# Kernel tuning notes

Hardware: AMD Instinct MI355X
Metric: run time of the kernel (lower is better)

The kernel has to match this reference:

```python
import jax, jax.numpy as jnp
import numpy as np

HID, HEADS, NL, WIN = 512, 4, 2, 5
DH = HID // HEADS
SLOPE = 0.2
EPS = 1e-5
B, L = 16, 1024
NEG_INF = -1e30


def _layer_norm(x, g, b):
    m = jnp.mean(x, axis=-1, keepdims=True)
    v = jnp.mean(jnp.square(x - m), axis=-1, keepdims=True)
    return (x - m) * jax.lax.rsqrt(v + EPS) * g + b


def _build_masks(attention_mask, last_starts, seq_len):
    # node layout: [g, h_1..h_T, l], total N = seq_len + 2
    bsz = attention_mask.shape[0]
    N = seq_len + 2
    pos = jnp.arange(N)
    last = last_starts[:, None, None]  # (B,1,1)
    global_mask = jnp.ones((bsz, 1, N), jnp.float32)
    # local node: g, itself, and tokens of the last utterance (node idx last+1 .. seq_len)
    local_mask = ((pos == 0) | (pos == N - 1) | ((pos >= last + 1) & (pos <= seq_len))).astype(jnp.float32)  # (B,1,N)
    # token nodes: global node + window of neighboring tokens
    ii = jnp.arange(seq_len)[:, None]          # query token index
    jj = jnp.arange(N)[None, :]                # key node index
    t = jj - 1                                 # token index of key node (valid in [0, seq_len))
    win = (t >= 0) & (t < seq_len) & (jnp.abs(ii - t) <= WIN)
    base = (jj == 0) | win                     # (L,N)
    # tokens at/after last utterance start also attend to the local node
    to_local = (jnp.arange(seq_len)[None, :, None] >= last_starts[:, None, None]) & (jj[None] == N - 1)  # (B,L,N)
    token_mask = (base[None] | to_local).astype(jnp.float32)
    # padding: key tokens masked by attention_mask; g and l always visible; padded queries fully masked
    ones_col = jnp.ones((bsz, seq_len, 1), jnp.float32)
    pad = jnp.concatenate([ones_col, jnp.broadcast_to(attention_mask[:, None, :], (bsz, seq_len, seq_len)), ones_col], axis=-1)
    token_mask = token_mask * pad * attention_mask[:, :, None]
    return global_mask, local_mask, token_mask


def _gat(q, kv, W, a, mask):
    # W: (hid, hid) as torch Linear weight (out,in); a: (H, 2*DH)
    bsz, Lq, _ = q.shape
    N = kv.shape[1]
    Q = (q @ W.T).reshape(bsz, Lq, HEADS, DH)
    K = (kv @ W.T).reshape(bsz, N, HEADS, DH)
    V = K  # key==value tensor in this module, same projection
    # additive score decomposes: (a . [Q||K]) = Q.a_q + K.a_k
    sq = jnp.einsum('bqhd,hd->bhq', Q, a[:, :DH])
    sk = jnp.einsum('bkhd,hd->bhk', K, a[:, DH:])
    s = sq[:, :, :, None] + sk[:, :, None, :]           # (B,H,Lq,N)
    s = jnp.where(s >= 0, s, SLOPE * s)                 # LeakyReLU
    s = jnp.where(mask[:, None, :, :] > 0, s, NEG_INF)
    w = jax.nn.softmax(s, axis=-1)
    w = jnp.where(jnp.isnan(w), 0.0, w)
    out = jnp.einsum('bhqk,bkhd->bqhd', w, V)
    return out.reshape(bsz, Lq, HID)


def setup_inputs() -> dict:
    key = jax.random.key(0)
    ks = jax.random.split(key, 10)
    scale = 1.0 / np.sqrt(HID)
    return {
        'global_embedding': jax.random.normal(ks[0], (B, HID), jnp.float32),
        'token_embeddings': jax.random.normal(ks[1], (B, L, HID), jnp.float32),
        'local_embedding': jax.random.normal(ks[2], (B, HID), jnp.float32),
        'attention_mask': jnp.ones((B, L), jnp.float32),
        'last_utterance_starts': jax.random.randint(ks[3], (B,), 0, 512, jnp.int32),
        'gat_W': jax.random.normal(ks[4], (NL, HID, HID), jnp.float32) * scale,
        'gat_a': jax.random.normal(ks[5], (NL, HEADS, 2 * DH), jnp.float32) * scale,
        'ln_gamma': jnp.ones((NL, HID), jnp.float32),
        'ln_beta': jnp.zeros((NL, HID), jnp.float32),
        'ffn_w1': jax.random.normal(ks[6], (3, HID, 4 * HID), jnp.float32) * scale,
        'ffn_b1': jnp.zeros((3, 4 * HID), jnp.float32),
        'ffn_w2': jax.random.normal(ks[7], (3, 4 * HID, HID), jnp.float32) * (1.0 / np.sqrt(4 * HID)),
        'ffn_b2': jnp.zeros((3, HID), jnp.float32),
        'out_ln_gamma': jnp.ones((3, HID), jnp.float32),
        'out_ln_beta': jnp.zeros((3, HID), jnp.float32),
    }


def reference(global_embedding, token_embeddings, local_embedding, attention_mask,
              last_utterance_starts, gat_W, gat_a, ln_gamma, ln_beta,
              ffn_w1, ffn_b1, ffn_w2, ffn_b2, out_ln_gamma, out_ln_beta):
    bsz, seq_len, _ = token_embeddings.shape
    gm, lm, tm = _build_masks(attention_mask, last_utterance_starts, seq_len)
    g = global_embedding[:, None, :]
    h = token_embeddings
    l = local_embedding[:, None, :]
    nodes = jnp.concatenate([g, h, l], axis=1)
    for k in range(NL):
        g_new = jax.nn.elu(_gat(g, nodes, gat_W[k], gat_a[k], gm))
        h_new = jax.nn.elu(_gat(h, nodes, gat_W[k], gat_a[k], tm))
        l_new = jax.nn.elu(_gat(l, nodes, gat_W[k], gat_a[k], lm))
        g = _layer_norm(g + g_new, ln_gamma[k], ln_beta[k])
        h = _layer_norm(h + h_new, ln_gamma[k], ln_beta[k])
        l = _layer_norm(l + l_new, ln_gamma[k], ln_beta[k])
        nodes = jnp.concatenate([g, h, l], axis=1)
    def ffn(x, i):
        hmid = jax.nn.gelu(x @ ffn_w1[i] + ffn_b1[i], approximate=False)
        return hmid @ ffn_w2[i] + ffn_b2[i]
    g = g + ffn(g, 0)
    h = h + ffn(h, 1)
    l = l + ffn(l, 2)
    updated_global = _layer_norm(g[:, 0], out_ln_gamma[0], out_ln_beta[0])
    updated_tokens = _layer_norm(h, out_ln_gamma[1], out_ln_beta[1])
    updated_local = _layer_norm(l[:, 0], out_ln_gamma[2], out_ln_beta[2])
    return updated_global, updated_tokens, updated_local
```

## Files before the change

### kernel.cpp

```cpp
#include <hip/hip_runtime.h>
#include <stdint.h>
#include <math.h>

#define HIDN 512
#define NHEAD 4
#define DHEAD 128
#define BATCH 16
#define SEQ 1024
#define NNODE 1026
#define MROWS (BATCH * NNODE)
#define MPAD 16512
#define MTOK (BATCH * SEQ)
#define FFD 2048
#define JCH 114

typedef short bf16x8 __attribute__((ext_vector_type(8)));
typedef float f32x4 __attribute__((ext_vector_type(4)));

__device__ __forceinline__ float bf2f(ushort u) {
    union { uint32_t i; float f; } v; v.i = ((uint32_t)u) << 16; return v.f;
}
__device__ __forceinline__ ushort f2bf(float f) {
    uint32_t x = __float_as_uint(f);
    return (ushort)((x + 0x7fffu + ((x >> 16) & 1u)) >> 16);
}
__device__ __forceinline__ float gelu(float v) {
    float z = v * 0.70710678118654752f;
    float az = fabsf(z);
    float t = __builtin_amdgcn_rcpf(1.f + 0.3275911f * az);
    float y = ((((1.061405429f * t - 1.453152027f) * t + 1.421413741f) * t
                - 0.284496736f) * t + 0.254829592f) * t;
    float e = __expf(-az * az);
    float erfv = 1.f - y * e;
    erfv = (z >= 0.f) ? erfv : -erfv;
    return 0.5f * v * (1.f + erfv);
}
__device__ __forceinline__ int cswz(int row, int col) {
    return row * 128 + ((((col >> 2) ^ (row & 7)) & 31) << 2) + (col & 3);
}

__global__ __launch_bounds__(256) void k_build_nodes(
    const float* __restrict__ g, const float* __restrict__ tok,
    const float* __restrict__ l, ushort* __restrict__ nb)
{
    int idx = blockIdx.x * 256 + threadIdx.x;
    int r = idx >> 9, c = idx & 511;
    float u = 0.f;
    if (r < MROWS) {
        int b = r / NNODE;
        int n = r - b * NNODE;
        if (n == 0)            u = g[b * HIDN + c];
        else if (n <= SEQ)     u = tok[((size_t)b * SEQ + (n - 1)) * HIDN + c];
        else                   u = l[b * HIDN + c];
    }
    nb[idx] = f2bf(u);
}

__global__ __launch_bounds__(256) void k_cvt(
    const float* __restrict__ in, ushort* __restrict__ out, int n)
{
    int idx = blockIdx.x * 256 + threadIdx.x;
    if (idx < n) out[idx] = f2bf(in[idx]);
}

__global__ __launch_bounds__(256) void k_transpose(
    const float* __restrict__ in, ushort* __restrict__ out, int R, int C)
{
    __shared__ float t[32][33];
    int x = blockIdx.x * 32 + threadIdx.x;
    int y0 = blockIdx.y * 32;
    for (int dy = threadIdx.y; dy < 32; dy += 8)
        t[dy][threadIdx.x] = in[(size_t)(y0 + dy) * C + x];
    __syncthreads();
    int ox = y0 + threadIdx.x;
    int oy0 = blockIdx.x * 32;
    for (int dy = threadIdx.y; dy < 32; dy += 8)
        out[(size_t)(oy0 + dy) * R + ox] = f2bf(t[threadIdx.x][dy]);
}

#define BM 128
#define BN 128
#define BK 64

__global__ __launch_bounds__(256) void k_gemm_bt(
    const ushort* __restrict__ A, const ushort* __restrict__ Bt,
    float* __restrict__ Cf, ushort* __restrict__ Cb,
    const float* __restrict__ bias,
    int N, int K, int ldb, int mode, int amap, int mguard, int first)
{
    __shared__ ushort smem[2 * (BM * BK + BN * BK)];
    int tid = threadIdx.x;
    int lane = tid & 63;
    int wave = tid >> 6;
    int wm = wave >> 1, wn = wave & 1;

    int GX = gridDim.x;
    int nwg = GX * gridDim.y;
    int bid = blockIdx.y * GX + blockIdx.x;
    int q = nwg >> 3, r = nwg & 7;
    int xcd = bid & 7, pos = bid >> 3;
    int cbase = (xcd < r) ? xcd * (q + 1) : r * (q + 1) + (xcd - r) * q;
    int wk = cbase + pos;
    int m0 = (wk / GX) * BM;
    int n0 = (wk % GX) * BN;

    f32x4 acc[4][4];
#pragma unroll
    for (int i = 0; i < 4; ++i)
#pragma unroll
        for (int j = 0; j < 4; ++j) acc[i][j] = (f32x4){0.f, 0.f, 0.f, 0.f};

    int lr = lane >> 3;
    int gco = ((lane & 7) ^ lr) * 8;

    const ushort* pA[4];
    const ushort* pB[4];
#pragma unroll
    for (int u = 0; u < 4; ++u) {
        int qq = wave * 4 + u;
        int rr8 = qq * 8 + lr;
        int grA = m0 + rr8;
        if (amap) grA = grA + 2 * (grA >> 10) + 1;
        pA[u] = A + (size_t)grA * K + gco;
        int grB = n0 + rr8;
        pB[u] = Bt + (size_t)grB * ldb + gco;
    }

    auto stage = [&](int buf) {
        ushort* sA = smem + buf * (BM * BK + BN * BK);
        ushort* sB = sA + BM * BK;
#pragma unroll
        for (int u = 0; u < 4; ++u) {
            int qq = wave * 4 + u;
            __builtin_amdgcn_global_load_lds(
                (const __attribute__((address_space(1))) void*)pA[u],
                (__attribute__((address_space(3))) void*)&sA[qq * 512], 16, 0, 0);
            __builtin_amdgcn_global_load_lds(
                (const __attribute__((address_space(1))) void*)pB[u],
                (__attribute__((address_space(3))) void*)&sB[qq * 512], 16, 0, 0);
            pA[u] += BK;
            pB[u] += BK;
        }
    };

    const int nk = K / BK;
    stage(0);
    __syncthreads();

    int rr = lane & 7;
    int rhi = (lane & 15) >> 3;
    for (int t = 0; t < nk; ++t) {
        if (t + 1 < nk) stage((t + 1) & 1);

        const ushort* sAr = smem + (t & 1) * (BM * BK + BN * BK);
        const ushort* sBr = sAr + BM * BK;
#pragma unroll
        for (int kk = 0; kk < BK; kk += 32) {
            int c4 = (kk >> 3) + (lane >> 4);
            int swz = rr * 64 + ((c4 ^ rr) << 3);
            bf16x8 af[4], bfr[4];
#pragma unroll
            for (int i = 0; i < 4; ++i)
                af[i] = *reinterpret_cast<const bf16x8*>(&sAr[(wm * 8 + i * 2 + rhi) * 512 + swz]);
#pragma unroll
            for (int j = 0; j < 4; ++j)
                bfr[j] = *reinterpret_cast<const bf16x8*>(&sBr[(wn * 8 + j * 2 + rhi) * 512 + swz]);
#pragma unroll
            for (int i = 0; i < 4; ++i)
#pragma unroll
                for (int j = 0; j < 4; ++j)
                    acc[i][j] = __builtin_amdgcn_mfma_f32_16x16x32_bf16(af[i], bfr[j], acc[i][j], 0, 0, 0);
        }
        asm volatile("s_waitcnt vmcnt(0)" ::: "memory");
        __builtin_amdgcn_s_barrier();
    }
    __syncthreads();

    float* sC = (float*)smem;
    int rb = (lane >> 4) * 4;
    int cb = lane & 15;
    int lrow = tid >> 2;
    int lcol = (tid & 3) << 5;
#pragma unroll
    for (int pass = 0; pass < 2; ++pass) {
        if (wm == pass) {
#pragma unroll
            for (int i = 0; i < 4; ++i)
#pragma unroll
                for (int j = 0; j < 4; ++j)
#pragma unroll
                    for (int rg = 0; rg < 4; ++rg)
                        sC[cswz(i * 16 + rb + rg, wn * 64 + j * 16 + cb)] = acc[i][j][rg];
        }
        __syncthreads();
        int gm = m0 + pass * 64 + lrow;
        if (gm < mguard) {
            int gn0 = n0 + lcol;
            float v[32];
#pragma unroll
            for (int e4 = 0; e4 < 8; ++e4) {
                float4 t = *(const float4*)&sC[cswz(lrow, lcol + e4 * 4)];
                v[e4 * 4 + 0] = t.x; v[e4 * 4 + 1] = t.y;
                v[e4 * 4 + 2] = t.z; v[e4 * 4 + 3] = t.w;
            }
            if (mode == 1 || mode == 3) {
                uint4* dst = (uint4*)(Cb + (size_t)gm * N + gn0);
#pragma unroll
                for (int q2 = 0; q2 < 4; ++q2) {
                    float s[8];
#pragma unroll
                    for (int t = 0; t < 8; ++t) {
                        float x = v[q2 * 8 + t];
                        s[t] = (mode == 1) ? gelu(x + bias[gn0 + q2 * 8 + t]) : x;
                    }
                    uint4 w;
                    w.x = (uint32_t)f2bf(s[0]) | ((uint32_t)f2bf(s[1]) << 16);
                    w.y = (uint32_t)f2bf(s[2]) | ((uint32_t)f2bf(s[3]) << 16);
                    w.z = (uint32_t)f2bf(s[4]) | ((uint32_t)f2bf(s[5]) << 16);
                    w.w = (uint32_t)f2bf(s[6]) | ((uint32_t)f2bf(s[7]) << 16);
                    dst[q2] = w;
                }
            } else {
                float4* dst = (float4*)(Cf + (size_t)gm * N + gn0);
#pragma unroll
                for (int e4 = 0; e4 < 8; ++e4) {
                    float4 t;
                    t.x = v[e4 * 4 + 0]; t.y = v[e4 * 4 + 1];
                    t.z = v[e4 * 4 + 2]; t.w = v[e4 * 4 + 3];
                    if (!first) {
                        float4 o = dst[e4];
                        t.x += o.x; t.y += o.y; t.z += o.z; t.w += o.w;
                    }
                    dst[e4] = t;
                }
            }
        }
        __syncthreads();
    }
}

__global__ __launch_bounds__(256) void k_sqsk(
    const ushort* __restrict__ P, const float* __restrict__ a,
    float* __restrict__ sq, float* __restrict__ sk)
{
    int wave = threadIdx.x >> 6, lane = threadIdx.x & 63;
    int row = blockIdx.x * 4 + wave;
    if (row >= MROWS) return;
    int hh = lane >> 4;
    int o0 = lane * 8;
    int dl = o0 & 127;
    const ushort* p = P + (size_t)row * HIDN + o0;
    const float* a1 = a + hh * 256 + dl;
    const float* a2 = a1 + 128;
    float s1 = 0.f, s2 = 0.f;
#pragma unroll
    for (int d = 0; d < 8; ++d) {
        float pv = bf2f(p[d]);
        s1 += pv * a1[d];
        s2 += pv * a2[d];
    }
#pragma unroll
    for (int off = 8; off; off >>= 1) {
        s1 += __shfl_xor(s1, off);
        s2 += __shfl_xor(s2, off);
    }
    if ((lane & 15) == 0) {
        sq[row * 4 + hh] = s1;
        sk[row * 4 + hh] = s2;
    }
}

__global__ __launch_bounds__(64) void k_attn_token(
    const ushort* __restrict__ P, const float* __restrict__ sq, const float* __restrict__ sk,
    const float* __restrict__ am, const int* __restrict__ last,
    const float* __restrict__ gam, const float* __restrict__ bet,
    ushort* __restrict__ nb)
{
    int bid = blockIdx.x;
    int tokid = ((bid & 7) << 11) | (bid >> 3);
    int b = tokid >> 10, i = tokid & 1023;
    int lane = threadIdx.x;
    int hh = lane >> 4;
    int base = b * NNODE;
    int qrow = base + 1 + i;

    int kr[13];
    int val[13];
    int rowok = am[b * SEQ + i] > 0.f ? 1 : 0;
    kr[0] = base; val[0] = rowok;
#pragma unroll
    for (int s = 0; s < 11; ++s) {
        int t = i - 5 + s;
        int inb = (t >= 0) && (t <= SEQ - 1);
        int tt = inb ? t : 0;
        int v = inb && rowok && (am[b * SEQ + tt] > 0.f);
        kr[1 + s] = base + 1 + tt;
        val[1 + s] = v;
    }
    kr[12] = base + SEQ + 1;
    val[12] = (rowok && (i >= last[b])) ? 1 : 0;

    float sqv = sq[qrow * 4 + hh];
    float sc[13];
    float mx = -1e30f;
#pragma unroll
    for (int t = 0; t < 13; ++t) {
        float s = 0.f;
        if (val[t]) {
            s = sqv + sk[kr[t] * 4 + hh];
            s = s >= 0.f ? s : 0.2f * s;
            mx = fmaxf(mx, s);
        }
        sc[t] = s;
    }
    float den = 0.f;
#pragma unroll
    for (int t = 0; t < 13; ++t) {
        float ev = 0.f;
        if (val[t]) ev = expf(sc[t] - mx);
        sc[t] = ev; den += ev;
    }
    float inv = (den > 1e-30f && den < 1e30f) ? 1.f / den : 0.f;

    int o0 = lane * 8;
    float accv[8] = {0.f, 0.f, 0.f, 0.f, 0.f, 0.f, 0.f, 0.f};
#pragma unroll
    for (int t = 0; t < 13; ++t) {
        if (val[t]) {
            float wgt = sc[t] * inv;
            const ushort* pv = P + (size_t)kr[t] * HIDN + o0;
#pragma unroll
            for (int d = 0; d < 8; ++d) accv[d] += wgt * bf2f(pv[d]);
        }
    }

    ushort* nrow = nb + (size_t)qrow * HIDN + o0;
    float x[8], s1 = 0.f, s2 = 0.f;
#pragma unroll
    for (int d = 0; d < 8; ++d) {
        float v = accv[d];
        v = v > 0.f ? v : expf(v) - 1.f;
        v += bf2f(nrow[d]);
        x[d] = v; s1 += v; s2 += v * v;
    }
#pragma unroll
    for (int off = 32; off; off >>= 1) { s1 += __shfl_xor(s1, off); s2 += __shfl_xor(s2, off); }
    float mean = s1 * (1.f / 512.f);
    float var = s2 * (1.f / 512.f) - mean * mean; var = fmaxf(var, 0.f);
    float rn = rsqrtf(var + 1e-5f);
#pragma unroll
    for (int d = 0; d < 8; ++d) {
        float y = (x[d] - mean) * rn * gam[o0 + d] + bet[o0 + d];
        nrow[d] = f2bf(y);
    }
}

__global__ __launch_bounds__(256) void k_glsm(
    const float* __restrict__ sq, const float* __restrict__ sk,
    const int* __restrict__ last,
    float* __restrict__ ebuf, float* __restrict__ einv)
{
    __shared__ float red[1024];
    int rw = blockIdx.x, b = rw >> 1, isl = rw & 1;
    int base = b * NNODE;
    int qrow = base + (isl ? (SEQ + 1) : 0);
    int lastb = last[b];
    int tid = threadIdx.x;

    float sqh[4];
#pragma unroll
    for (int h = 0; h < 4; ++h) sqh[h] = sq[qrow * 4 + h];

    float mx[4] = {-1e30f, -1e30f, -1e30f, -1e30f};
    for (int j = tid; j < NNODE; j += 256) {
        bool ok = !isl || (j == 0 || j == SEQ + 1 || (j >= lastb + 1 && j <= SEQ));
        if (ok) {
#pragma unroll
            for (int h = 0; h < 4; ++h) {
                float s = sqh[h] + sk[(base + j) * 4 + h];
                s = s >= 0.f ? s : 0.2f * s;
                mx[h] = fmaxf(mx[h], s);
            }
        }
    }
#pragma unroll
    for (int h = 0; h < 4; ++h) red[tid * 4 + h] = mx[h];
    __syncthreads();
    for (int s = 128; s; s >>= 1) {
        if (tid < s) {
#pragma unroll
            for (int h = 0; h < 4; ++h)
                red[tid * 4 + h] = fmaxf(red[tid * 4 + h], red[(tid + s) * 4 + h]);
        }
        __syncthreads();
    }
#pragma unroll
    for (int h = 0; h < 4; ++h) mx[h] = red[h];
    __syncthreads();

    float sm[4] = {0.f, 0.f, 0.f, 0.f};
    for (int j = tid; j < NNODE; j += 256) {
        bool ok = !isl || (j == 0 || j == SEQ + 1 || (j >= lastb + 1 && j <= SEQ));
#pragma unroll
        for (int h = 0; h < 4; ++h) {
            float v = 0.f;
            if (ok) {
                float s = sqh[h] + sk[(base + j) * 4 + h];
                s = s >= 0.f ? s : 0.2f * s;
                v = expf(s - mx[h]);
            }
            ebuf[((size_t)rw * NNODE + j) * 4 + h] = v;
            sm[h] += v;
        }
    }
#pragma unroll
    for (int h = 0; h < 4; ++h) red[tid * 4 + h] = sm[h];
    __syncthreads();
    for (int s = 128; s; s >>= 1) {
        if (tid < s) {
#pragma unroll
            for (int h = 0; h < 4; ++h) red[tid * 4 + h] += red[(tid + s) * 4 + h];
        }
        __syncthreads();
    }
    if (tid < 4) {
        float den = red[tid];
        einv[rw * 4 + tid] = (den > 1e-30f && den < 1e30f) ? 1.f / den : 0.f;
    }
}

__global__ __launch_bounds__(256) void k_glpv(
    const ushort* __restrict__ P, const float* __restrict__ ebuf,
    float* __restrict__ pout2)
{
    __shared__ float es[JCH * 4];
    int p = blockIdx.x, rw = blockIdx.y;
    int b = rw >> 1;
    int base = b * NNODE;
    int tid = threadIdx.x;
    for (int t = tid; t < JCH * 4; t += 256)
        es[t] = ebuf[((size_t)rw * NNODE + p * JCH) * 4 + t];
    __syncthreads();
    int o0 = tid, o1 = tid + 256;
    int h0 = o0 >> 7, h1 = o1 >> 7;
    const ushort* Pb = P + (size_t)(base + p * JCH) * HIDN;
    float a0 = 0.f, a1 = 0.f;
    for (int j = 0; j < JCH; ++j) {
        const ushort* pr = Pb + (size_t)j * HIDN;
        a0 += es[j * 4 + h0] * bf2f(pr[o0]);
        a1 += es[j * 4 + h1] * bf2f(pr[o1]);
    }
    float* o = pout2 + ((size_t)rw * 9 + p) * HIDN;
    o[o0] = a0;
    o[o1] = a1;
}

__global__ __launch_bounds__(256) void k_glred(
    const float* __restrict__ pout2, const float* __restrict__ einv,
    const float* __restrict__ gam, const float* __restrict__ bet,
    ushort* __restrict__ nb)
{
    __shared__ float red[512];
    int rw = blockIdx.x, b = rw >> 1, isl = rw & 1;
    size_t qrow = (size_t)b * NNODE + (isl ? SEQ + 1 : 0);
    int tid = threadIdx.x;
    float xv[2], s1 = 0.f, s2 = 0.f;
#pragma unroll
    for (int u = 0; u < 2; ++u) {
        int o = tid + u * 256;
        int h = o >> 7;
        float acc = 0.f;
#pragma unroll
        for (int p = 0; p < 9; ++p)
            acc += pout2[((size_t)rw * 9 + p) * HIDN + o];
        acc *= einv[rw * 4 + h];
        float v = acc > 0.f ? acc : expf(acc) - 1.f;
        v += bf2f(nb[qrow * HIDN + o]);
        xv[u] = v; s1 += v; s2 += v * v;
    }
    red[tid] = s1;
    __syncthreads();
    for (int s = 128; s; s >>= 1) { if (tid < s) red[tid] += red[tid + s]; __syncthreads(); }
    float mean = red[0] * (1.f / 512.f);
    __syncthreads();
    red[tid] = s2;
    __syncthreads();
    for (int s = 128; s; s >>= 1) { if (tid < s) red[tid] += red[tid + s]; __syncthreads(); }
    float var = red[0] * (1.f / 512.f) - mean * mean; var = fmaxf(var, 0.f);
    float rn = rsqrtf(var + 1e-5f);
#pragma unroll
    for (int u = 0; u < 2; ++u) {
        int o = tid + u * 256;
        float y = (xv[u] - mean) * rn * gam[o] + bet[o];
        nb[qrow * HIDN + o] = f2bf(y);
    }
}

__global__ __launch_bounds__(256) void k_fgl1(
    const ushort* __restrict__ nb, const float* __restrict__ w1,
    float* __restrict__ pmid)
{
    __shared__ float xs[64];
    int p = blockIdx.x, rw = blockIdx.y;
    int b = rw >> 1, isl = rw & 1;
    int idx = isl ? 2 : 0;
    size_t nrow = (size_t)b * NNODE + (isl ? SEQ + 1 : 0);
    int tid = threadIdx.x;
    if (tid < 64) xs[tid] = bf2f(nb[nrow * HIDN + p * 64 + tid]);
    __syncthreads();
    const float* W1 = w1 + (size_t)idx * HIDN * FFD + (size_t)p * 64 * FFD;
    float acc[8] = {0.f, 0.f, 0.f, 0.f, 0.f, 0.f, 0.f, 0.f};
    for (int ii = 0; ii < 64; ++ii) {
        float xv = xs[ii];
        const float* wrow = W1 + (size_t)ii * FFD + tid;
#pragma unroll
        for (int u = 0; u < 8; ++u) acc[u] += xv * wrow[u * 256];
    }
    float* o = pmid + ((size_t)rw * 8 + p) * FFD + tid;
#pragma unroll
    for (int u = 0; u < 8; ++u) o[u * 256] = acc[u];
}

__global__ __launch_bounds__(256) void k_fgl2(
    const float* __restrict__ pmid, const float* __restrict__ b1,
    float* __restrict__ mid)
{
    int g = blockIdx.x * 256 + threadIdx.x;
    int e4 = g * 4;
    int rw = e4 >> 11;
    int m = e4 & 2047;
    int isl = rw & 1;
    int idx = isl ? 2 : 0;
#pragma unroll
    for (int d = 0; d < 4; ++d) {
        float s = 0.f;
#pragma unroll
        for (int p = 0; p < 8; ++p)
            s += pmid[((size_t)rw * 8 + p) * FFD + m + d];
        s += b1[idx * FFD + m + d];
        mid[(size_t)rw * FFD + m + d] = gelu(s);
    }
}

__global__ __launch_bounds__(256) void k_fgl3(
    const float* __restrict__ mid, const float* __restrict__ w2,
    float* __restrict__ pout)
{
    __shared__ float ms[256];
    int p = blockIdx.x, rw = blockIdx.y;
    int isl = rw & 1;
    int idx = isl ? 2 : 0;
    int tid = threadIdx.x;
    ms[tid] = mid[(size_t)rw * FFD + p * 256 + tid];
    __syncthreads();
    const float* W2 = w2 + (size_t)idx * FFD * HIDN + (size_t)p * 256 * HIDN;
    float a0 = 0.f, a1 = 0.f;
    for (int mm = 0; mm < 256; ++mm) {
        float mv = ms[mm];
        const float* wrow = W2 + (size_t)mm * HIDN + tid;
        a0 += mv * wrow[0];
        a1 += mv * wrow[256];
    }
    float* o = pout + ((size_t)rw * 8 + p) * HIDN + tid;
    o[0] = a0;
    o[256] = a1;
}

__global__ __launch_bounds__(256) void k_fgl4(
    const float* __restrict__ pout, const float* __restrict__ b2,
    const ushort* __restrict__ nb,
    const float* __restrict__ og, const float* __restrict__ obt,
    float* __restrict__ out)
{
    __shared__ float red[512];
    int rw = blockIdx.x;
    int b = rw >> 1, isl = rw & 1;
    int idx = isl ? 2 : 0;
    size_t nrow = (size_t)b * NNODE + (isl ? SEQ + 1 : 0);
    int tid = threadIdx.x;
    float xv[2], s1 = 0.f, s2 = 0.f;
#pragma unroll
    for (int u = 0; u < 2; ++u) {
        int o = tid + u * 256;
        float s = 0.f;
#pragma unroll
        for (int p = 0; p < 8; ++p)
            s += pout[((size_t)rw * 8 + p) * HIDN + o];
        s += b2[idx * HIDN + o] + bf2f(nb[nrow * HIDN + o]);
        xv[u] = s; s1 += s; s2 += s * s;
    }
    red[tid] = s1;
    __syncthreads();
    for (int s = 128; s; s >>= 1) { if (tid < s) red[tid] += red[tid + s]; __syncthreads(); }
    float mean = red[0] * (1.f / 512.f);
    __syncthreads();
    red[tid] = s2;
    __syncthreads();
    for (int s = 128; s; s >>= 1) { if (tid < s) red[tid] += red[tid + s]; __syncthreads(); }
    float var = red[0] * (1.f / 512.f) - mean * mean; var = fmaxf(var, 0.f);
    float rn = rsqrtf(var + 1e-5f);
    size_t obase = isl ? ((size_t)8192 + (size_t)MTOK * HIDN + (size_t)b * HIDN)
                       : ((size_t)b * HIDN);
#pragma unroll
    for (int u = 0; u < 2; ++u) {
        int o = tid + u * 256;
        out[obase + o] = (xv[u] - mean) * rn * og[idx * HIDN + o] + obt[idx * HIDN + o];
    }
}

__global__ __launch_bounds__(64) void k_ln_final(
    float* __restrict__ Pt, const ushort* __restrict__ nb,
    const float* __restrict__ b2,
    const float* __restrict__ gam, const float* __restrict__ bet)
{
    int r = blockIdx.x, lane = threadIdx.x;
    int nrow = r + 2 * (r >> 10) + 1;
    int o0 = lane * 8;
    float* x = Pt + (size_t)r * HIDN + o0;
    const ushort* res = nb + (size_t)nrow * HIDN + o0;
    float v[8], s1 = 0.f, s2 = 0.f;
#pragma unroll
    for (int d = 0; d < 8; ++d) {
        float t = x[d] + b2[o0 + d] + bf2f(res[d]);
        v[d] = t; s1 += t; s2 += t * t;
    }
#pragma unroll
    for (int off = 32; off; off >>= 1) { s1 += __shfl_xor(s1, off); s2 += __shfl_xor(s2, off); }
    float mean = s1 * (1.f / 512.f);
    float var = s2 * (1.f / 512.f) - mean * mean; var = fmaxf(var, 0.f);
    float rn = rsqrtf(var + 1e-5f);
#pragma unroll
    for (int d = 0; d < 8; ++d)
        x[d] = (v[d] - mean) * rn * gam[o0 + d] + bet[o0 + d];
}

extern "C" void kernel_launch(void* const* d_in, const int* in_sizes, int n_in,
                              void* d_out, int out_size, void* d_ws, size_t ws_size,
                              hipStream_t stream)
{
    (void)in_sizes; (void)n_in; (void)out_size; (void)ws_size;
    const float* g_emb   = (const float*)d_in[0];
    const float* tok_emb = (const float*)d_in[1];
    const float* l_emb   = (const float*)d_in[2];
    const float* am      = (const float*)d_in[3];
    const int*   last    = (const int*)d_in[4];
    const float* gat_W   = (const float*)d_in[5];
    const float* gat_a   = (const float*)d_in[6];
    const float* ln_g    = (const float*)d_in[7];
    const float* ln_b    = (const float*)d_in[8];
    const float* ffn_w1  = (const float*)d_in[9];
    const float* ffn_b1  = (const float*)d_in[10];
    const float* ffn_w2  = (const float*)d_in[11];
    const float* ffn_b2  = (const float*)d_in[12];
    const float* oln_g   = (const float*)d_in[13];
    const float* oln_b   = (const float*)d_in[14];
    float* out = (float*)d_out;

    char* w = (char*)d_ws;
    ushort* nodes_b = (ushort*)w; w += (size_t)MPAD * HIDN * 2;
    char*   scratch = w;          w += (size_t)8 * 1024 * 1024;
    ushort* w1t     = (ushort*)w; w += (size_t)FFD * HIDN * 2;
    ushort* w2t     = (ushort*)w; w += (size_t)FFD * HIDN * 2;
    ushort* gatWb   = (ushort*)w; w += (size_t)2 * HIDN * HIDN * 2;
    float*  sqb     = (float*)w;  w += (size_t)MPAD * 4 * 4;
    float*  skb     = (float*)w;  w += (size_t)MPAD * 4 * 4;
    ushort* Hmid    = (ushort*)w; w += (size_t)MTOK * FFD * 2;

    float* pmid = (float*)scratch;
    float* mid  = pmid + (size_t)32 * 8 * FFD;
    float* pout = mid + (size_t)32 * FFD;
    float* ebuf  = (float*)(scratch + (size_t)3 * 1024 * 1024);
    float* einv  = ebuf + (size_t)32 * NNODE * 4;
    float* pout2 = einv + 128;

    ushort* P = (ushort*)out;
    float* Pt = out + 8192;

    k_build_nodes<<<MPAD * HIDN / 256, 256, 0, stream>>>(g_emb, tok_emb, l_emb, nodes_b);
    k_cvt<<<(2 * HIDN * HIDN) / 256, 256, 0, stream>>>(gat_W, gatWb, 2 * HIDN * HIDN);
    k_transpose<<<dim3(FFD / 32, HIDN / 32), dim3(32, 8), 0, stream>>>(ffn_w1 + (size_t)HIDN * FFD, w1t, HIDN, FFD);
    k_transpose<<<dim3(HIDN / 32, FFD / 32), dim3(32, 8), 0, stream>>>(ffn_w2 + (size_t)FFD * HIDN, w2t, FFD, HIDN);

    for (int k = 0; k < 2; ++k) {
        k_gemm_bt<<<dim3(HIDN / BN, MPAD / BM), 256, 0, stream>>>(
            nodes_b, gatWb + (size_t)k * HIDN * HIDN, nullptr, P, nullptr,
            HIDN, HIDN, HIDN, 3, 0, MROWS, 1);
        k_sqsk<<<MROWS / 4, 256, 0, stream>>>(P, gat_a + k * NHEAD * 2 * DHEAD, sqb, skb);
        k_attn_token<<<MTOK, 64, 0, stream>>>(P, sqb, skb, am, last,
                                              ln_g + k * HIDN, ln_b + k * HIDN, nodes_b);
        k_glsm<<<32, 256, 0, stream>>>(sqb, skb, last, ebuf, einv);
        k_glpv<<<dim3(9, 32), 256, 0, stream>>>(P, ebuf, pout2);
        k_glred<<<32, 256, 0, stream>>>(pout2, einv, ln_g + k * HIDN, ln_b + k * HIDN, nodes_b);
    }

    k_fgl1<<<dim3(8, 32), 256, 0, stream>>>(nodes_b, ffn_w1, pmid);
    k_fgl2<<<64, 256, 0, stream>>>(pmid, ffn_b1, mid);
    k_fgl3<<<dim3(8, 32), 256, 0, stream>>>(mid, ffn_w2, pout);
    k_fgl4<<<32, 256, 0, stream>>>(pout, ffn_b2, nodes_b, oln_g, oln_b, out);

    k_gemm_bt<<<dim3(FFD / BN, MTOK / BM), 256, 0, stream>>>(
        nodes_b, w1t, nullptr, Hmid,
        ffn_b1 + FFD, FFD, HIDN, HIDN, 1, 1, MTOK, 1);
    k_gemm_bt<<<dim3(HIDN / BN, MTOK / BM), 256, 0, stream>>>(
        Hmid, w2t, Pt, nullptr, nullptr,
        HIDN, FFD, FFD, 0, 0, MTOK, 1);
    k_ln_final<<<MTOK, 64, 0, stream>>>(Pt, nodes_b, ffn_b2 + HIDN, oln_g + HIDN, oln_b + HIDN);
}
```

Measured before the change: 489.6 us.

## Fuse GAT score projections into GEMM epilogue and shrink K tile to 32

Removes the separate k_sqsk kernel. The GAT projection GEMM's epilogue now computes the per-head sq/sk dot products with the attention vector directly from the fp32 accumulators and writes them out. This saves a full re-read of the projected node matrix and one launch per layer. In the same change the GEMM K tile is cut from 64 to 32, with a new LDS swizzle and staging layout. That halves shared memory use but doubles the number of K iterations and barriers in every GEMM, including the large FFN ones. The sk output is assumed to sit at a fixed offset after sqb, which must match how skb is allocated.

```diff
diff --git a/kernel.cpp b/kernel.cpp
--- a/kernel.cpp
+++ b/kernel.cpp
@@ -80,7 +80,7 @@
 
 #define BM 128
 #define BN 128
-#define BK 64
+#define BK 32
 
 __global__ __launch_bounds__(256) void k_gemm_bt(
     const ushort* __restrict__ A, const ushort* __restrict__ Bt,
@@ -110,19 +110,18 @@
 #pragma unroll
         for (int j = 0; j < 4; ++j) acc[i][j] = (f32x4){0.f, 0.f, 0.f, 0.f};
 
-    int lr = lane >> 3;
-    int gco = ((lane & 7) ^ lr) * 8;
-
-    const ushort* pA[4];
-    const ushort* pB[4];
-#pragma unroll
-    for (int u = 0; u < 4; ++u) {
-        int qq = wave * 4 + u;
-        int rr8 = qq * 8 + lr;
-        int grA = m0 + rr8;
+    int srow = lane >> 2;
+    int gco = (((lane & 3) ^ (srow & 3)) << 3);
+
+    const ushort* pA[2];
+    const ushort* pB[2];
+#pragma unroll
+    for (int u = 0; u < 2; ++u) {
+        int g = wave * 2 + u;
+        int grA = m0 + g * 16 + srow;
         if (amap) grA = grA + 2 * (grA >> 10) + 1;
         pA[u] = A + (size_t)grA * K + gco;
-        int grB = n0 + rr8;
+        int grB = n0 + g * 16 + srow;
         pB[u] = Bt + (size_t)grB * ldb + gco;
     }
 
@@ -130,14 +129,14 @@
         ushort* sA = smem + buf * (BM * BK + BN * BK);
         ushort* sB = sA + BM * BK;
 #pragma unroll
-        for (int u = 0; u < 4; ++u) {
-            int qq = wave * 4 + u;
+        for (int u = 0; u < 2; ++u) {
+            int g = wave * 2 + u;
             __builtin_amdgcn_global_load_lds(
                 (const __attribute__((address_space(1))) void*)pA[u],
-                (__attribute__((address_space(3))) void*)&sA[qq * 512], 16, 0, 0);
+                (__attribute__((address_space(3))) void*)&sA[g * 512], 16, 0, 0);
             __builtin_amdgcn_global_load_lds(
                 (const __attribute__((address_space(1))) void*)pB[u],
-                (__attribute__((address_space(3))) void*)&sB[qq * 512], 16, 0, 0);
+                (__attribute__((address_space(3))) void*)&sB[g * 512], 16, 0, 0);
             pA[u] += BK;
             pB[u] += BK;
         }
@@ -149,28 +148,27 @@
 
     int rr = lane & 7;
     int rhi = (lane & 15) >> 3;
+    int co = (((lane >> 4) ^ (lane & 3)) << 3);
     for (int t = 0; t < nk; ++t) {
         if (t + 1 < nk) stage((t + 1) & 1);
 
         const ushort* sAr = smem + (t & 1) * (BM * BK + BN * BK);
         const ushort* sBr = sAr + BM * BK;
-#pragma unroll
-        for (int kk = 0; kk < BK; kk += 32) {
-            int c4 = (kk >> 3) + (lane >> 4);
-            int swz = rr * 64 + ((c4 ^ rr) << 3);
-            bf16x8 af[4], bfr[4];
-#pragma unroll
-            for (int i = 0; i < 4; ++i)
-                af[i] = *reinterpret_cast<const bf16x8*>(&sAr[(wm * 8 + i * 2 + rhi) * 512 + swz]);
+        bf16x8 af[4], bfr[4];
+#pragma unroll
+        for (int i = 0; i < 4; ++i)
+            af[i] = *reinterpret_cast<const bf16x8*>(
+                &sAr[(wm * 64 + i * 16 + rhi * 8 + rr) * 32 + co]);
+#pragma unroll
+        for (int j = 0; j < 4; ++j)
+            bfr[j] = *reinterpret_cast<const bf16x8*>(
+                &sBr[(wn * 64 + j * 16 + rhi * 8 + rr) * 32 + co]);
+#pragma unroll
+        for (int i = 0; i < 4; ++i)
 #pragma unroll
             for (int j = 0; j < 4; ++j)
-                bfr[j] = *reinterpret_cast<const bf16x8*>(&sBr[(wn * 8 + j * 2 + rhi) * 512 + swz]);
-#pragma unroll
-            for (int i = 0; i < 4; ++i)
-#pragma unroll
-                for (int j = 0; j < 4; ++j)
-                    acc[i][j] = __builtin_amdgcn_mfma_f32_16x16x32_bf16(af[i], bfr[j], acc[i][j], 0, 0, 0);
-        }
+                acc[i][j] = __builtin_amdgcn_mfma_f32_16x16x32_bf16(af[i], bfr[j], acc[i][j], 0, 0, 0);
+
         asm volatile("s_waitcnt vmcnt(0)" ::: "memory");
         __builtin_amdgcn_s_barrier();
     }
@@ -204,6 +202,22 @@
                 v[e4 * 4 + 2] = t.z; v[e4 * 4 + 3] = t.w;
             }
             if (mode == 1 || mode == 3) {
+                if (mode == 3) {
+                    const float* a1 = bias + (gn0 >> 7) * 256 + (gn0 & 127);
+                    const float* a2 = a1 + 128;
+                    float s1 = 0.f, s2 = 0.f;
+#pragma unroll
+                    for (int j = 0; j < 32; ++j) {
+                        s1 += v[j] * a1[j];
+                        s2 += v[j] * a2[j];
+                    }
+                    s1 += __shfl_xor(s1, 1); s1 += __shfl_xor(s1, 2);
+                    s2 += __shfl_xor(s2, 1); s2 += __shfl_xor(s2, 2);
+                    if ((tid & 3) == 0) {
+                        Cf[gm * 4 + (gn0 >> 7)] = s1;
+                        Cf[(size_t)MPAD * 4 + gm * 4 + (gn0 >> 7)] = s2;
+                    }
+                }
                 uint4* dst = (uint4*)(Cb + (size_t)gm * N + gn0);
 #pragma unroll
                 for (int q2 = 0; q2 < 4; ++q2) {
@@ -236,37 +250,6 @@
             }
         }
         __syncthreads();
-    }
-}
-
-__global__ __launch_bounds__(256) void k_sqsk(
-    const ushort* __restrict__ P, const float* __restrict__ a,
-    float* __restrict__ sq, float* __restrict__ sk)
-{
-    int wave = threadIdx.x >> 6, lane = threadIdx.x & 63;
-    int row = blockIdx.x * 4 + wave;
-    if (row >= MROWS) return;
-    int hh = lane >> 4;
-    int o0 = lane * 8;
-    int dl = o0 & 127;
-    const ushort* p = P + (size_t)row * HIDN + o0;
-    const float* a1 = a + hh * 256 + dl;
-    const float* a2 = a1 + 128;
-    float s1 = 0.f, s2 = 0.f;
-#pragma unroll
-    for (int d = 0; d < 8; ++d) {
-        float pv = bf2f(p[d]);
-        s1 += pv * a1[d];
-        s2 += pv * a2[d];
-    }
-#pragma unroll
-    for (int off = 8; off; off >>= 1) {
-        s1 += __shfl_xor(s1, off);
-        s2 += __shfl_xor(s2, off);
-    }
-    if ((lane & 15) == 0) {
-        sq[row * 4 + hh] = s1;
-        sk[row * 4 + hh] = s2;
     }
 }
 
@@ -683,9 +666,9 @@
 
     for (int k = 0; k < 2; ++k) {
         k_gemm_bt<<<dim3(HIDN / BN, MPAD / BM), 256, 0, stream>>>(
-            nodes_b, gatWb + (size_t)k * HIDN * HIDN, nullptr, P, nullptr,
+            nodes_b, gatWb + (size_t)k * HIDN * HIDN, sqb, P,
+            gat_a + k * NHEAD * 2 * DHEAD,
             HIDN, HIDN, HIDN, 3, 0, MROWS, 1);
-        k_sqsk<<<MROWS / 4, 256, 0, stream>>>(P, gat_a + k * NHEAD * 2 * DHEAD, sqb, skb);
         k_attn_token<<<MTOK, 64, 0, stream>>>(P, sqb, skb, am, last,
                                               ln_g + k * HIDN, ln_b + k * HIDN, nodes_b);
         k_glsm<<<32, 256, 0, stream>>>(sqb, skb, last, ebuf, einv);
```

Result: slower. 508.0 us (+3.7%).
